# Optimization experiments

Hardware: AMD Instinct MI355X
Metric: run time of the kernel (lower is better)

The kernel has to match this reference:

```python
import jax, jax.numpy as jnp
import numpy as np

NB, H, C = 6, 4, 192
B, S, L = 2, 64, 256
VOCAB, ED = 24, 64


def setup_inputs() -> dict:
    key = jax.random.key(0)
    ks = iter(jax.random.split(key, 32))
    r = lambda sh: jax.random.normal(next(ks), sh, jnp.float32) * 0.02
    z = lambda sh: jnp.zeros(sh, jnp.float32)
    return {
        'tokens': jax.random.randint(next(ks), (B, S, L), 0, VOCAB, jnp.int32),
        'emb': r((VOCAB, ED)),
        'proj_w': r((C, ED)), 'proj_b': z((C,)),
        'ln_g': jnp.ones((NB, 3, C), jnp.float32), 'ln_b': z((NB, 3, C)),
        'wq': r((NB, 2, C, C)), 'wk': r((NB, 2, C, C)),
        'wv': r((NB, 2, C, C)), 'wo': r((NB, 2, C, C)),
        'bq': z((NB, 2, C)), 'bk': z((NB, 2, C)),
        'bv': z((NB, 2, C)), 'bo': z((NB, 2, C)),
        'ffn_w1': r((NB, 4 * C, C)), 'ffn_b1': z((NB, 4 * C)),
        'ffn_w2': r((NB, C, 4 * C)), 'ffn_b2': z((NB, C)),
        'pw_w': r((C,)), 'pw_b': z(()),
    }


def rotary(x):
    # ESM-style rotary embedding over positions along dim -2, feature dim last.
    d = x.shape[-1]
    inv = 1.0 / (10000.0 ** (jnp.arange(0, d, 2, dtype=jnp.float32) / d))
    t = jnp.arange(x.shape[-2], dtype=jnp.float32)
    f = t[:, None] * inv[None, :]                  # (pos, d/2)
    emb = jnp.concatenate([f, f], axis=-1)         # (pos, d)
    cos, sin = jnp.cos(emb), jnp.sin(emb)
    x1, x2 = jnp.split(x, 2, axis=-1)
    return x * cos + jnp.concatenate([-x2, x1], axis=-1) * sin


def ln_ch(x, g, b, eps=1e-5):
    # LayerNorm over channel axis 1 of (B,C,X,Y) (== transpose->LN->transpose).
    m = x.mean(axis=1, keepdims=True)
    v = jnp.var(x, axis=1, keepdims=True)
    return (x - m) * jax.lax.rsqrt(v + eps) * g[None, :, None, None] + b[None, :, None, None]


def lin_attn(x, wq, wk, wv, wo, bq, bk, bv, bo):
    # ScaledLinearAttention: elu+1 feature map, attends over dim -2 of (B,A,N,C).
    Bm, A, N, Cm = x.shape
    dh = Cm // H
    sh = lambda t: t.reshape(Bm, A, N, H, dh).transpose(0, 1, 3, 2, 4)  # (B,A,H,N,dh)
    q = sh(x @ wq.T + bq)
    k = sh(x @ wk.T + bk)
    v = sh(x @ wv.T + bv)
    q = (jax.nn.elu(q) + 1.0) / jnp.sqrt(jnp.float32(dh))
    k = jax.nn.elu(k) + 1.0
    kv = jnp.einsum('bahnd,bahne->bahde', k, v)
    z = 1.0 / (jnp.einsum('bahnd,bahd->bahn', q, k.sum(axis=-2)) + 1e-6)
    o = jnp.einsum('bahnd,bahde->bahne', q, kv) * z[..., None]
    o = o.transpose(0, 1, 3, 2, 4).reshape(Bm, A, N, Cm)
    return o @ wo.T + bo


def fwd(tokens, emb, proj_w, proj_b, ln_g, ln_b, wq, wk, wv, wo, bq, bk, bv, bo,
        ffn_w1, ffn_b1, ffn_w2, ffn_b2, pw_w, pw_b):
    x = emb[tokens]                    # (B,S,L,ED)
    x = x @ proj_w.T + proj_b          # (B,S,L,C)
    x = rotary(x)                      # rotary over L positions
    out = jnp.transpose(x, (0, 3, 1, 2))  # (B,C,S,L)
    for i in range(NB):
        # row attention (over L)
        h = ln_ch(out, ln_g[i, 0], ln_b[i, 0])
        h = jnp.transpose(h, (0, 2, 3, 1))  # (B,S,L,C)
        h = lin_attn(h, wq[i, 0], wk[i, 0], wv[i, 0], wo[i, 0],
                     bq[i, 0], bk[i, 0], bv[i, 0], bo[i, 0])
        out = out + jnp.transpose(h, (0, 3, 1, 2))
        # col attention (over S)
        h = ln_ch(out, ln_g[i, 1], ln_b[i, 1])
        h = jnp.transpose(h, (0, 3, 2, 1))  # (B,L,S,C)
        h = lin_attn(h, wq[i, 1], wk[i, 1], wv[i, 1], wo[i, 1],
                     bq[i, 1], bk[i, 1], bv[i, 1], bo[i, 1])
        out = out + jnp.transpose(h, (0, 3, 2, 1))
        # 1x1-conv FFN
        h = ln_ch(out, ln_g[i, 2], ln_b[i, 2])
        h = jnp.einsum('bcxy,oc->boxy', h, ffn_w1[i]) + ffn_b1[i][None, :, None, None]
        h = jax.nn.gelu(h, approximate=False)
        h = jnp.einsum('bcxy,oc->boxy', h, ffn_w2[i]) + ffn_b2[i][None, :, None, None]
        out = out + h
    o = jnp.einsum('bcxy,c->bxy', out, pw_w) + pw_b   # pwFNN 1x1 conv to 1 ch
    return jax.nn.sigmoid(jax.nn.softplus(o))


def reference(tokens, emb, proj_w, proj_b, ln_g, ln_b, wq, wk, wv, wo, bq, bk, bv, bo,
              ffn_w1, ffn_b1, ffn_w2, ffn_b2, pw_w, pw_b):
    return fwd(tokens, emb, proj_w, proj_b, ln_g, ln_b, wq, wk, wv, wo, bq, bk, bv, bo,
               ffn_w1, ffn_b1, ffn_w2, ffn_b2, pw_w, pw_b)
```

## Files before the change

### kernel.cpp

```cpp
#include <hip/hip_runtime.h>
#include <hip/hip_bf16.h>
#include <math.h>

#define NBLK 6
#define NH 4
#define CCH 192
#define BB 2
#define SS 64
#define LL 256
#define DH 48
#define NP (BB*SS*LL)
#define BUF ((size_t)NP*CCH)

typedef __attribute__((ext_vector_type(8))) short short8;
typedef __attribute__((ext_vector_type(4))) float float4v;
typedef __attribute__((ext_vector_type(2))) unsigned int uintx2;

__device__ __forceinline__ unsigned short f2b(float f) {
    union { float f; unsigned int u; } v; v.f = f;
    unsigned int r = v.u + 0x7FFF + ((v.u >> 16) & 1);
    return (unsigned short)(r >> 16);
}
__device__ __forceinline__ float b2f(unsigned short u) {
    union { unsigned int u; float f; } v; v.u = ((unsigned int)u) << 16;
    return v.f;
}
__device__ __forceinline__ unsigned int cvt_pk_bf16(float lo, float hi) {
    unsigned int r;
    asm("v_cvt_pk_bf16_f32 %0, %1, %2" : "=v"(r) : "v"(lo), "v"(hi));
    return r;
}
__device__ __forceinline__ void st2u(unsigned short* p0, unsigned short* p1, float a, float b) {
    unsigned int u = cvt_pk_bf16(a, b);
    *p0 = (unsigned short)u;
    *p1 = (unsigned short)(u >> 16);
}
__device__ __forceinline__ void xf_unpack(uintx2 u, float* f) {
    union { unsigned int x; float ff; } t;
    t.x = u[0] << 16;          f[0] = t.ff;
    t.x = u[0] & 0xffff0000u;  f[1] = t.ff;
    t.x = u[1] << 16;          f[2] = t.ff;
    t.x = u[1] & 0xffff0000u;  f[3] = t.ff;
}
__device__ __forceinline__ float gelu_f(float v) {
    float z = v * 0.7071067811865475f;
    float a = fabsf(z);
    float t = __builtin_amdgcn_rcpf(fmaf(0.3275911f, a, 1.0f));
    float p = fmaf(t, 1.061405429f, -1.453152027f);
    p = fmaf(t, p, 1.421413741f);
    p = fmaf(t, p, -0.284496736f);
    p = fmaf(t, p, 0.254829592f);
    p *= t;
    float e = __expf(-a * a);
    float er = fmaf(-p, e, 1.0f);
    er = __builtin_copysignf(er, z);
    return 0.5f * v * (1.0f + er);
}
__device__ __forceinline__ void async_lds16(const void* g, void* l) {
    __builtin_amdgcn_global_load_lds(
        (const __attribute__((address_space(1))) unsigned int*)g,
        (__attribute__((address_space(3))) unsigned int*)l, 16, 0, 0);
}

#define XF(p16, c) (((size_t)(p16) * 192 + (c)) << 4)

template<int N, int K>
__global__ void swz_conv(const float* __restrict__ src, unsigned short* __restrict__ dst, int layers) {
    int s = blockIdx.x * 256 + threadIdx.x;
    if (s >= layers * N * K) return;
    int li = s / (N * K);
    int t = s - li * (N * K);
    constexpr int KC = K / 32;
    int chunk = t >> 9, c = t & 511;
    int g = chunk / KC, sk = chunk - g * KC;
    int lane = c >> 3, ko = c & 7;
    int n = g * 16 + (lane & 15), k = sk * 32 + (lane >> 4) * 8 + ko;
    dst[s] = f2b(src[(size_t)li * N * K + (size_t)n * K + k]);
}
__global__ void wqkv_swz(const float* __restrict__ wq, const float* __restrict__ wk,
                         const float* __restrict__ wv, unsigned short* __restrict__ d) {
    int s = blockIdx.x * 256 + threadIdx.x;
    int wi = s / (576 * 192);
    int t = s - wi * 576 * 192;
    int chunk = t >> 9, c = t & 511;
    int g = chunk / 6, sk = chunk - g * 6;
    int lane = c >> 3, ko = c & 7;
    int n = g * 16 + (lane & 15), k = sk * 32 + (lane >> 4) * 8 + ko;
    int sg = n / 192, row = n - sg * 192;
    const float* src = (sg == 0) ? wq : (sg == 1) ? wk : wv;
    d[s] = f2b(src[(size_t)wi * 192 * 192 + (size_t)row * 192 + k]);
}
__global__ void bqkv_concat(const float* __restrict__ bq, const float* __restrict__ bk,
                            const float* __restrict__ bv, float* __restrict__ d) {
    int idx = blockIdx.x * 256 + threadIdx.x;
    if (idx >= NBLK * 2 * 576) return;
    int wi = idx / 576, n = idx - (idx / 576) * 576;
    int sg = n / 192, row = n - sg * 192;
    const float* src = (sg == 0) ? bq : (sg == 1) ? bk : bv;
    d[idx] = src[wi * CCH + row];
}

__global__ void gather_kernel(const int* __restrict__ tokens, const float* __restrict__ emb,
                              unsigned short* __restrict__ Eg) {
    int idx = blockIdx.x * 256 + threadIdx.x;
    int p = idx >> 6, c = idx & 63;
    Eg[idx] = f2b(emb[tokens[p] * 64 + c]);
}

__global__ __launch_bounds__(256) void rotary_ln_kernel(const float* __restrict__ Xt,
                                                        unsigned short* __restrict__ X,
                                                        unsigned short* __restrict__ Hn,
                                                        const float* __restrict__ g, const float* __restrict__ b) {
    int wave = threadIdx.x >> 6;
    int lane = threadIdx.x & 63;
    int p = blockIdx.x * 4 + wave;
    int l = p & (LL - 1);
    const float* xp = Xt + (size_t)p * CCH;
    float v[3];
    #pragma unroll
    for (int i = 0; i < 3; ++i) {
        int c = lane + i * 64;
        int j = c % 96;
        float inv = expf((float)(2 * j) * (-9.210340371976184f / 192.0f));
        float ang = (float)l * inv;
        float part = (c < 96) ? -xp[c + 96] : xp[c - 96];
        v[i] = xp[c] * cosf(ang) + part * sinf(ang);
    }
    float s = v[0] + v[1] + v[2];
    float qq = v[0] * v[0] + v[1] * v[1] + v[2] * v[2];
    #pragma unroll
    for (int off = 32; off; off >>= 1) {
        s += __shfl_xor(s, off, 64);
        qq += __shfl_xor(qq, off, 64);
    }
    float mean = s * (1.0f / 192.0f);
    float var = qq * (1.0f / 192.0f) - mean * mean;
    float r = rsqrtf(var + 1e-5f);
    unsigned short* hp = Hn + (size_t)p * CCH;
    const int p16 = p >> 4, pr = p & 15;
    #pragma unroll
    for (int i = 0; i < 3; ++i) {
        int c = lane + i * 64;
        X[XF(p16, c) + pr] = f2b(v[i]);
        hp[c] = f2b((v[i] - mean) * r * g[c] + b[c]);
    }
}

template<int MT, int EPI>
__global__ __launch_bounds__(256, (MT == 128) ? 3 : 4)
void mm192(const unsigned short* __restrict__ A, const unsigned short* __restrict__ Wsw,
           const float* __restrict__ bias,
           unsigned short* __restrict__ O0, unsigned short* __restrict__ O1,
           unsigned short* __restrict__ O2,
           float* __restrict__ Of,
           int M, int N, int K) {
    constexpr int NI = MT / 32;
    __shared__ __align__(16) unsigned char lds[(MT == 128) ? 51200 : 28672];
    const int tid = threadIdx.x;
    const int lane = tid & 63;
    const int w = tid >> 6;
    const int wm = w >> 1, wn = w & 1;
    const int m0 = blockIdx.y * MT;
    const int g0 = blockIdx.x * 12;
    const int q = lane >> 4;
    const int q8 = q << 3;
    const int r15 = lane & 15;
    const int KC = K >> 5;

    for (int c = w; c < (MT / 16) * KC; c += 4) {
        int g = c / KC, sk = c - g * KC;
        async_lds16(A + (size_t)(m0 + g * 16 + r15) * K + sk * 32 + q8, lds + c * 1024);
    }

    float4v acc[NI][6];
    #pragma unroll
    for (int i = 0; i < NI; ++i)
        #pragma unroll
        for (int j = 0; j < 6; ++j)
            acc[i][j] = (float4v){0.f, 0.f, 0.f, 0.f};

    __syncthreads();

    for (int sk = 0; sk < KC; ++sk) {
        short8 af[NI], wf[6];
        #pragma unroll
        for (int j = 0; j < 6; ++j)
            wf[j] = *(const short8*)(Wsw + (((size_t)(g0 + wn * 6 + j) * KC + sk) << 9) + lane * 8);
        #pragma unroll
        for (int i = 0; i < NI; ++i)
            af[i] = *(const short8*)(lds + (((wm * NI + i) * KC + sk) << 10) + lane * 16);
        #pragma unroll
        for (int i = 0; i < NI; ++i)
            #pragma unroll
            for (int j = 0; j < 6; ++j)
                acc[i][j] = __builtin_amdgcn_mfma_f32_16x16x32_bf16(af[i], wf[j], acc[i][j], 0, 0, 0);
    }

    const int nb = blockIdx.x * 192 + wn * 96 + r15;
    const int mb = m0 + wm * (MT / 2) + q * 4;

    if (EPI == 0) {
        const int bx = blockIdx.x;
        unsigned short* dst = (bx == 0) ? O0 : (bx == 1) ? O1 : O2;
        #pragma unroll
        for (int j = 0; j < 6; ++j) {
            int n = nb + j * 16;
            int col = wn * 96 + j * 16 + r15;
            float bv = bias[n];
            #pragma unroll
            for (int i = 0; i < NI; ++i) {
                int mrow = wm * (MT / 2) + i * 16 + q * 4;
                #pragma unroll
                for (int r = 0; r < 4; ++r) {
                    float v = acc[i][j][r] + bv;
                    if (bx < 2) v = (v > 0.f) ? v + 1.f : __expf(v);
                    if (bx == 0) v *= 0.14433756729740643f;
                    dst[(size_t)(m0 + mrow + r) * 192 + col] = f2b(v);
                }
            }
        }
    } else {
        #pragma unroll
        for (int j = 0; j < 6; ++j) {
            int n = nb + j * 16;
            float bv = bias[n];
            #pragma unroll
            for (int i = 0; i < NI; ++i) {
                int mrow = mb + i * 16;
                #pragma unroll
                for (int r = 0; r < 4; ++r)
                    Of[(size_t)(mrow + r) * N + n] = acc[i][j][r] + bv;
            }
        }
    }
}


__global__ __launch_bounds__(256, 4)
void wo_qkv(const unsigned short* __restrict__ Ho,
            const unsigned short* __restrict__ WOs, const float* __restrict__ BO,
            unsigned short* __restrict__ Xres,
            const float* __restrict__ lng, const float* __restrict__ lnb,
            const unsigned short* __restrict__ QKVs, const float* __restrict__ bqkv,
            unsigned short* __restrict__ Qb, unsigned short* __restrict__ Kb,
            unsigned short* __restrict__ Vb) {
    __shared__ __align__(16) unsigned char lds[25600];
    unsigned char* Lo = lds;
    float* lsum = (float*)(lds + 12288);
    float* lsq  = lsum + 128;
    unsigned char* Ap = lds + 13312;
    const int tid = threadIdx.x;
    const int lane = tid & 63;
    const int w = tid >> 6;
    const int m0 = blockIdx.x * 32;
    const int q = lane >> 4, q8 = q << 3, r15 = lane & 15;
    const int nb = w * 48 + r15;

    #pragma unroll
    for (int it = 0; it < 3; ++it) {
        int c = it * 4 + w;
        int g = c / 6, sk = c - g * 6;
        async_lds16(Ho + (size_t)(m0 + g * 16 + r15) * 192 + sk * 32 + q8, Lo + c * 1024);
    }
    __syncthreads();

    float4v acc[2][3];
    #pragma unroll
    for (int i = 0; i < 2; ++i)
        #pragma unroll
        for (int j = 0; j < 3; ++j)
            acc[i][j] = (float4v){0.f, 0.f, 0.f, 0.f};
    #pragma unroll
    for (int kk = 0; kk < 6; ++kk) {
        short8 af[2], wf[3];
        #pragma unroll
        for (int j = 0; j < 3; ++j)
            wf[j] = *(const short8*)(WOs + (((size_t)(w * 3 + j) * 6 + kk) << 9) + lane * 8);
        #pragma unroll
        for (int i = 0; i < 2; ++i)
            af[i] = *(const short8*)(Lo + ((i * 6 + kk) << 10) + lane * 16);
        #pragma unroll
        for (int i = 0; i < 2; ++i)
            #pragma unroll
            for (int j = 0; j < 3; ++j)
                acc[i][j] = __builtin_amdgcn_mfma_f32_16x16x32_bf16(af[i], wf[j], acc[i][j], 0, 0, 0);
    }

    #pragma unroll
    for (int j = 0; j < 3; ++j) {
        int n = nb + j * 16;
        float bv = BO[n];
        #pragma unroll
        for (int i = 0; i < 2; ++i) {
            unsigned short* xp = Xres + XF(blockIdx.x * 2 + i, n) + q * 4;
            uintx2 u = *(const uintx2*)xp;
            float f[4]; xf_unpack(u, f);
            #pragma unroll
            for (int r = 0; r < 4; ++r) acc[i][j][r] += bv + f[r];
            uintx2 o;
            o[0] = cvt_pk_bf16(acc[i][j][0], acc[i][j][1]);
            o[1] = cvt_pk_bf16(acc[i][j][2], acc[i][j][3]);
            *(uintx2*)xp = o;
        }
    }
    #pragma unroll
    for (int i = 0; i < 2; ++i)
        #pragma unroll
        for (int r = 0; r < 4; ++r) {
            float s1 = acc[i][0][r] + acc[i][1][r] + acc[i][2][r];
            float s2 = acc[i][0][r] * acc[i][0][r] + acc[i][1][r] * acc[i][1][r] + acc[i][2][r] * acc[i][2][r];
            #pragma unroll
            for (int off = 1; off < 16; off <<= 1) {
                s1 += __shfl_xor(s1, off, 64);
                s2 += __shfl_xor(s2, off, 64);
            }
            if (r15 == 0) {
                int rl = i * 16 + q * 4 + r;
                lsum[rl * 4 + w] = s1;
                lsq[rl * 4 + w] = s2;
            }
        }
    __syncthreads();
    #pragma unroll
    for (int i = 0; i < 2; ++i) {
        float mean[4], rstd[4];
        #pragma unroll
        for (int r = 0; r < 4; ++r) {
            int rl4 = (i * 16 + q * 4 + r) * 4;
            float s  = lsum[rl4] + lsum[rl4 + 1] + lsum[rl4 + 2] + lsum[rl4 + 3];
            float ss = lsq[rl4] + lsq[rl4 + 1] + lsq[rl4 + 2] + lsq[rl4 + 3];
            float m = s * (1.0f / 192.0f);
            mean[r] = m;
            rstd[r] = rsqrtf(ss * (1.0f / 192.0f) - m * m + 1e-5f);
        }
        #pragma unroll
        for (int j = 0; j < 3; ++j) {
            int h = nb + j * 16;
            float gg = lng[h], bb = lnb[h];
            unsigned short* ap = (unsigned short*)Ap + (i * 6 + (h >> 5)) * 512
                               + ((h >> 3) & 3) * 128 + (h & 7) + q * 32;
            float v0 = (acc[i][j][0] - mean[0]) * rstd[0] * gg + bb;
            float v1 = (acc[i][j][1] - mean[1]) * rstd[1] * gg + bb;
            float v2 = (acc[i][j][2] - mean[2]) * rstd[2] * gg + bb;
            float v3 = (acc[i][j][3] - mean[3]) * rstd[3] * gg + bb;
            st2u(ap, ap + 8, v0, v1);
            st2u(ap + 16, ap + 24, v2, v3);
        }
    }
    __syncthreads();

    for (int seg = 0; seg < 3; ++seg) {
        float4v a2[2][3];
        #pragma unroll
        for (int i = 0; i < 2; ++i)
            #pragma unroll
            for (int j = 0; j < 3; ++j)
                a2[i][j] = (float4v){0.f, 0.f, 0.f, 0.f};
        #pragma unroll
        for (int kk = 0; kk < 6; ++kk) {
            short8 af[2], wf[3];
            #pragma unroll
            for (int j = 0; j < 3; ++j)
                wf[j] = *(const short8*)(QKVs + (((size_t)(seg * 12 + w * 3 + j) * 6 + kk) << 9) + lane * 8);
            #pragma unroll
            for (int i = 0; i < 2; ++i)
                af[i] = *(const short8*)(Ap + ((i * 6 + kk) << 10) + lane * 16);
            #pragma unroll
            for (int i = 0; i < 2; ++i)
                #pragma unroll
                for (int j = 0; j < 3; ++j)
                    a2[i][j] = __builtin_amdgcn_mfma_f32_16x16x32_bf16(af[i], wf[j], a2[i][j], 0, 0, 0);
        }
        unsigned short* dst = (seg == 0) ? Qb : (seg == 1) ? Kb : Vb;
        #pragma unroll
        for (int j = 0; j < 3; ++j) {
            int n = nb + j * 16;
            float bv = bqkv[seg * 192 + n];
            #pragma unroll
            for (int i = 0; i < 2; ++i) {
                int mrow = m0 + i * 16 + q * 4;
                #pragma unroll
                for (int r = 0; r < 4; ++r) {
                    float x = a2[i][j][r] + bv;
                    if (seg < 2) x = (x > 0.f) ? x + 1.f : __expf(x);
                    if (seg == 0) x *= 0.14433756729740643f;
                    dst[(size_t)(mrow + r) * 192 + n] = f2b(x);
                }
            }
        }
    }
}

template<bool LASTB>
__global__ __launch_bounds__(256, 2)
void wo_ffn_qkv(const unsigned short* __restrict__ Ho,
                const unsigned short* __restrict__ WOs, const float* __restrict__ BO,
                unsigned short* __restrict__ Xres,
                const float* __restrict__ ln1g, const float* __restrict__ ln1b,
                const unsigned short* __restrict__ W1s, const float* __restrict__ B1,
                const unsigned short* __restrict__ W2s, const float* __restrict__ B2,
                const float* __restrict__ ln2g, const float* __restrict__ ln2b,
                const unsigned short* __restrict__ QKVs, const float* __restrict__ bqkv,
                unsigned short* __restrict__ Qb, unsigned short* __restrict__ Kb,
                unsigned short* __restrict__ Vb) {
    __shared__ __align__(16) unsigned char lds[51200];
    unsigned char* Lo = lds;
    float* lsum = (float*)(lds + 24576);
    float* lsq  = lsum + 256;
    unsigned char* Ap = lds + 26624;
    const int tid = threadIdx.x;
    const int lane = tid & 63;
    const int w = tid >> 6;
    const int m0 = blockIdx.x * 64;
    const int q = lane >> 4, q8 = q << 3, r15 = lane & 15;
    const int nb = w * 48 + r15;

    #pragma unroll
    for (int it = 0; it < 6; ++it) {
        int c = it * 4 + w;
        int g = c / 6, sk = c - g * 6;
        async_lds16(Ho + (size_t)(m0 + g * 16 + r15) * 192 + sk * 32 + q8, Lo + c * 1024);
    }
    __syncthreads();

    float4v xres[4][3];
    #pragma unroll
    for (int i = 0; i < 4; ++i)
        #pragma unroll
        for (int j = 0; j < 3; ++j)
            xres[i][j] = (float4v){0.f, 0.f, 0.f, 0.f};
    #pragma unroll
    for (int kk = 0; kk < 6; ++kk) {
        short8 af[4], wf[3];
        #pragma unroll
        for (int j = 0; j < 3; ++j)
            wf[j] = *(const short8*)(WOs + (((size_t)(w * 3 + j) * 6 + kk) << 9) + lane * 8);
        #pragma unroll
        for (int i = 0; i < 4; ++i)
            af[i] = *(const short8*)(Lo + ((i * 6 + kk) << 10) + lane * 16);
        #pragma unroll
        for (int i = 0; i < 4; ++i)
            #pragma unroll
            for (int j = 0; j < 3; ++j)
                xres[i][j] = __builtin_amdgcn_mfma_f32_16x16x32_bf16(af[i], wf[j], xres[i][j], 0, 0, 0);
    }
    #pragma unroll
    for (int j = 0; j < 3; ++j) {
        int n = nb + j * 16;
        float bv = BO[n];
        #pragma unroll
        for (int i = 0; i < 4; ++i) {
            const unsigned short* xp = Xres + XF(blockIdx.x * 4 + i, n) + q * 4;
            uintx2 u = *(const uintx2*)xp;
            float f[4]; xf_unpack(u, f);
            #pragma unroll
            for (int r = 0; r < 4; ++r) xres[i][j][r] += bv + f[r];
        }
    }
    #pragma unroll
    for (int i = 0; i < 4; ++i)
        #pragma unroll
        for (int r = 0; r < 4; ++r) {
            float s1 = xres[i][0][r] + xres[i][1][r] + xres[i][2][r];
            float s2 = xres[i][0][r] * xres[i][0][r] + xres[i][1][r] * xres[i][1][r] + xres[i][2][r] * xres[i][2][r];
            #pragma unroll
            for (int off = 1; off < 16; off <<= 1) {
                s1 += __shfl_xor(s1, off, 64);
                s2 += __shfl_xor(s2, off, 64);
            }
            if (r15 == 0) {
                int rl = i * 16 + q * 4 + r;
                lsum[rl * 4 + w] = s1;
                lsq[rl * 4 + w] = s2;
            }
        }
    __syncthreads();
    #pragma unroll
    for (int i = 0; i < 4; ++i) {
        float mean[4], rstd[4];
        #pragma unroll
        for (int r = 0; r < 4; ++r) {
            int rl4 = (i * 16 + q * 4 + r) * 4;
            float s  = lsum[rl4] + lsum[rl4 + 1] + lsum[rl4 + 2] + lsum[rl4 + 3];
            float ss = lsq[rl4] + lsq[rl4 + 1] + lsq[rl4 + 2] + lsq[rl4 + 3];
            float m = s * (1.0f / 192.0f);
            mean[r] = m;
            rstd[r] = rsqrtf(ss * (1.0f / 192.0f) - m * m + 1e-5f);
        }
        #pragma unroll
        for (int j = 0; j < 3; ++j) {
            int h = nb + j * 16;
            float gg = ln1g[h], bb = ln1b[h];
            unsigned short* ap = (unsigned short*)Ap + (i * 6 + (h >> 5)) * 512
                               + ((h >> 3) & 3) * 128 + (h & 7) + q * 32;
            float v0 = (xres[i][j][0] - mean[0]) * rstd[0] * gg + bb;
            float v1 = (xres[i][j][1] - mean[1]) * rstd[1] * gg + bb;
            float v2 = (xres[i][j][2] - mean[2]) * rstd[2] * gg + bb;
            float v3 = (xres[i][j][3] - mean[3]) * rstd[3] * gg + bb;
            st2u(ap, ap + 8, v0, v1);
            st2u(ap + 16, ap + 24, v2, v3);
        }
    }
    __syncthreads();

    float4v acc2[4][3];
    #pragma unroll
    for (int i = 0; i < 4; ++i)
        #pragma unroll
        for (int j = 0; j < 3; ++j)
            acc2[i][j] = (float4v){0.f, 0.f, 0.f, 0.f};
    for (int hc = 0; hc < 4; ++hc) {
        float4v acc1[4][3];
        #pragma unroll
        for (int i = 0; i < 4; ++i)
            #pragma unroll
            for (int j = 0; j < 3; ++j)
                acc1[i][j] = (float4v){0.f, 0.f, 0.f, 0.f};
        #pragma unroll
        for (int kk = 0; kk < 6; ++kk) {
            short8 af[4], wf[3];
            #pragma unroll
            for (int j = 0; j < 3; ++j)
                wf[j] = *(const short8*)(W1s + (((size_t)(hc * 12 + w * 3 + j) * 6 + kk) << 9) + lane * 8);
            #pragma unroll
            for (int i = 0; i < 4; ++i)
                af[i] = *(const short8*)(Ap + ((i * 6 + kk) << 10) + lane * 16);
            #pragma unroll
            for (int i = 0; i < 4; ++i)
                #pragma unroll
                for (int j = 0; j < 3; ++j)
                    acc1[i][j] = __builtin_amdgcn_mfma_f32_16x16x32_bf16(af[i], wf[j], acc1[i][j], 0, 0, 0);
        }
        __syncthreads();
        #pragma unroll
        for (int i = 0; i < 4; ++i)
            #pragma unroll
            for (int j = 0; j < 3; ++j) {
                int h = nb + j * 16;
                float bv = B1[hc * 192 + h];
                unsigned short* lp = (unsigned short*)Lo + (i * 6 + (h >> 5)) * 512
                                   + ((h >> 3) & 3) * 128 + (h & 7) + q * 32;
                float v0 = gelu_f(acc1[i][j][0] + bv);
                float v1 = gelu_f(acc1[i][j][1] + bv);
                float v2 = gelu_f(acc1[i][j][2] + bv);
                float v3 = gelu_f(acc1[i][j][3] + bv);
                st2u(lp, lp + 8, v0, v1);
                st2u(lp + 16, lp + 24, v2, v3);
            }
        __syncthreads();
        #pragma unroll
        for (int kk = 0; kk < 6; ++kk) {
            short8 af[4], wf[3];
            #pragma unroll
            for (int j = 0; j < 3; ++j)
                wf[j] = *(const short8*)(W2s + (((size_t)(w * 3 + j) * 24 + hc * 6 + kk) << 9) + lane * 8);
            #pragma unroll
            for (int i = 0; i < 4; ++i)
                af[i] = *(const short8*)(Lo + ((i * 6 + kk) << 10) + lane * 16);
            #pragma unroll
            for (int i = 0; i < 4; ++i)
                #pragma unroll
                for (int j = 0; j < 3; ++j)
                    acc2[i][j] = __builtin_amdgcn_mfma_f32_16x16x32_bf16(af[i], wf[j], acc2[i][j], 0, 0, 0);
        }
    }

    #pragma unroll
    for (int j = 0; j < 3; ++j) {
        int n = nb + j * 16;
        float bv = B2[n];
        #pragma unroll
        for (int i = 0; i < 4; ++i) {
            #pragma unroll
            for (int r = 0; r < 4; ++r)
                xres[i][j][r] += acc2[i][j][r] + bv;
            unsigned short* xp = Xres + XF(blockIdx.x * 4 + i, n) + q * 4;
            uintx2 o;
            o[0] = cvt_pk_bf16(xres[i][j][0], xres[i][j][1]);
            o[1] = cvt_pk_bf16(xres[i][j][2], xres[i][j][3]);
            *(uintx2*)xp = o;
        }
    }
    if (LASTB) return;

    #pragma unroll
    for (int i = 0; i < 4; ++i)
        #pragma unroll
        for (int r = 0; r < 4; ++r) {
            float s1 = xres[i][0][r] + xres[i][1][r] + xres[i][2][r];
            float s2 = xres[i][0][r] * xres[i][0][r] + xres[i][1][r] * xres[i][1][r] + xres[i][2][r] * xres[i][2][r];
            #pragma unroll
            for (int off = 1; off < 16; off <<= 1) {
                s1 += __shfl_xor(s1, off, 64);
                s2 += __shfl_xor(s2, off, 64);
            }
            if (r15 == 0) {
                int rl = i * 16 + q * 4 + r;
                lsum[rl * 4 + w] = s1;
                lsq[rl * 4 + w] = s2;
            }
        }
    __syncthreads();
    #pragma unroll
    for (int i = 0; i < 4; ++i) {
        float mean[4], rstd[4];
        #pragma unroll
        for (int r = 0; r < 4; ++r) {
            int rl4 = (i * 16 + q * 4 + r) * 4;
            float s  = lsum[rl4] + lsum[rl4 + 1] + lsum[rl4 + 2] + lsum[rl4 + 3];
            float ss = lsq[rl4] + lsq[rl4 + 1] + lsq[rl4 + 2] + lsq[rl4 + 3];
            float m = s * (1.0f / 192.0f);
            mean[r] = m;
            rstd[r] = rsqrtf(ss * (1.0f / 192.0f) - m * m + 1e-5f);
        }
        #pragma unroll
        for (int j = 0; j < 3; ++j) {
            int h = nb + j * 16;
            float gg = ln2g[h], bb = ln2b[h];
            unsigned short* ap = (unsigned short*)Ap + (i * 6 + (h >> 5)) * 512
                               + ((h >> 3) & 3) * 128 + (h & 7) + q * 32;
            float v0 = (xres[i][j][0] - mean[0]) * rstd[0] * gg + bb;
            float v1 = (xres[i][j][1] - mean[1]) * rstd[1] * gg + bb;
            float v2 = (xres[i][j][2] - mean[2]) * rstd[2] * gg + bb;
            float v3 = (xres[i][j][3] - mean[3]) * rstd[3] * gg + bb;
            st2u(ap, ap + 8, v0, v1);
            st2u(ap + 16, ap + 24, v2, v3);
        }
    }
    __syncthreads();

    for (int seg = 0; seg < 3; ++seg) {
        float4v a2[4][3];
        #pragma unroll
        for (int i = 0; i < 4; ++i)
            #pragma unroll
            for (int j = 0; j < 3; ++j)
                a2[i][j] = (float4v){0.f, 0.f, 0.f, 0.f};
        #pragma unroll
        for (int kk = 0; kk < 6; ++kk) {
            short8 af[4], wf[3];
            #pragma unroll
            for (int j = 0; j < 3; ++j)
                wf[j] = *(const short8*)(QKVs + (((size_t)(seg * 12 + w * 3 + j) * 6 + kk) << 9) + lane * 8);
            #pragma unroll
            for (int i = 0; i < 4; ++i)
                af[i] = *(const short8*)(Ap + ((i * 6 + kk) << 10) + lane * 16);
            #pragma unroll
            for (int i = 0; i < 4; ++i)
                #pragma unroll
                for (int j = 0; j < 3; ++j)
                    a2[i][j] = __builtin_amdgcn_mfma_f32_16x16x32_bf16(af[i], wf[j], a2[i][j], 0, 0, 0);
        }
        unsigned short* dst = (seg == 0) ? Qb : (seg == 1) ? Kb : Vb;
        #pragma unroll
        for (int j = 0; j < 3; ++j) {
            int n = nb + j * 16;
            float bv = bqkv[seg * 192 + n];
            #pragma unroll
            for (int i = 0; i < 4; ++i) {
                int mrow = m0 + i * 16 + q * 4;
                #pragma unroll
                for (int r = 0; r < 4; ++r) {
                    float x = a2[i][j][r] + bv;
                    if (seg < 2) x = (x > 0.f) ? x + 1.f : __expf(x);
                    if (seg == 0) x *= 0.14433756729740643f;
                    dst[(size_t)(mrow + r) * 192 + n] = f2b(x);
                }
            }
        }
    }
}

__global__ __launch_bounds__(512) void attn_row8(const unsigned short* __restrict__ Qb,
                                                 const unsigned short* __restrict__ Kb,
                                                 const unsigned short* __restrict__ Vb,
                                                 unsigned short* __restrict__ O) {
    __shared__ __align__(16) unsigned char lds[100352];
    unsigned char* kvb = lds;
    float* kvsum = (float*)(lds + 51200);
    unsigned short* kvs = (unsigned short*)lds;
    const int tid = threadIdx.x;
    const int lane = tid & 63;
    const int w = tid >> 6;
    const int h = w & 3;
    const int half = w >> 2;
    const int q = lane >> 4, r15 = lane & 15, q8 = q * 8;
    const size_t base = (size_t)blockIdx.x * 256;

    short8 onesf;
    #pragma unroll
    for (int e = 0; e < 8; ++e) onesf[e] = (short)0x3F80;

    float4v kv[3][4];
    #pragma unroll
    for (int i = 0; i < 3; ++i)
        #pragma unroll
        for (int j = 0; j < 4; ++j)
            kv[i][j] = (float4v){0.f, 0.f, 0.f, 0.f};

    for (int ks = 0; ks < 128; ks += 32) {
        #pragma unroll
        for (int it = 0; it < 6; ++it) {
            int cc = it * 512 + tid;
            int gr = cc / 48, c8 = cc - gr * 48;
            int hf = gr >> 5, row = gr & 31;
            size_t poff = (base + (size_t)(ks + hf * 128 + row)) * 192;
            const unsigned short* gp = (c8 < 24) ? (Kb + poff + c8 * 8) : (Vb + poff + (c8 - 24) * 8);
            int ba = hf * 25600 + ((row * 800 + c8 * 16) ^ (((row >> 3) & 3) << 5));
            *(short8*)(kvb + ba) = *(const short8*)gp;
        }
        __syncthreads();
        short8 af[3], bf[3];
        const unsigned char* hb = kvb + half * 25600;
        #pragma unroll
        for (int t = 0; t < 3; ++t) {
            #pragma unroll
            for (int j = 0; j < 8; ++j) {
                int row = q8 + j;
                int sw = ((row >> 3) & 3) << 5;
                af[t][j] = *(const short*)(hb + ((row * 800 + (h * 48 + t * 16 + r15) * 2) ^ sw));
                bf[t][j] = *(const short*)(hb + ((row * 800 + 384 + (h * 48 + t * 16 + r15) * 2) ^ sw));
            }
        }
        #pragma unroll
        for (int i = 0; i < 3; ++i) {
            #pragma unroll
            for (int j = 0; j < 3; ++j)
                kv[i][j] = __builtin_amdgcn_mfma_f32_16x16x32_bf16(af[i], bf[j], kv[i][j], 0, 0, 0);
            kv[i][3] = __builtin_amdgcn_mfma_f32_16x16x32_bf16(af[i], onesf, kv[i][3], 0, 0, 0);
        }
        __syncthreads();
    }

    if (half) {
        float* kp = kvsum + h * 3072;
        #pragma unroll
        for (int i = 0; i < 3; ++i)
            #pragma unroll
            for (int j = 0; j < 4; ++j)
                #pragma unroll
                for (int r = 0; r < 4; ++r)
                    kp[((i * 4 + j) * 4 + r) * 64 + lane] = kv[i][j][r];
    }
    __syncthreads();
    if (!half) {
        const float* kp = kvsum + h * 3072;
        #pragma unroll
        for (int i = 0; i < 3; ++i)
            #pragma unroll
            for (int j = 0; j < 4; ++j)
                #pragma unroll
                for (int r = 0; r < 4; ++r)
                    kv[i][j][r] += kp[((i * 4 + j) * 4 + r) * 64 + lane];
        unsigned int* kz = (unsigned int*)(kvs + h * 4608);
        #pragma unroll
        for (int ii = 0; ii < 36; ++ii) kz[lane + ii * 64] = 0;
        #pragma unroll
        for (int i = 0; i < 3; ++i) {
            #pragma unroll
            for (int j = 0; j < 3; ++j)
                #pragma unroll
                for (int r = 0; r < 4; ++r)
                    kvs[(h * 64 + j * 16 + r15) * 72 + i * 16 + q * 4 + r] = f2b(kv[i][j][r]);
            if (r15 == 0)
                #pragma unroll
                for (int r = 0; r < 4; ++r)
                    kvs[(h * 64 + 48) * 72 + i * 16 + q * 4 + r] = f2b(kv[i][3][r]);
        }
    }
    __syncthreads();

    short8 bkv[2][4];
    #pragma unroll
    for (int kk = 0; kk < 2; ++kk)
        #pragma unroll
        for (int t = 0; t < 4; ++t)
            bkv[kk][t] = *(const short8*)&kvs[(h * 64 + t * 16 + r15) * 72 + kk * 32 + q8];

    for (int mt = half * 8; mt < half * 8 + 8; ++mt) {
        float4v o[4];
        #pragma unroll
        for (int t = 0; t < 4; ++t) o[t] = (float4v){0.f, 0.f, 0.f, 0.f};
        #pragma unroll
        for (int kk = 0; kk < 2; ++kk) {
            const unsigned short* qp = Qb + (base + (size_t)(mt * 16 + r15)) * 192
                                       + h * 48 + kk * 32 + q8;
            short8 aq = *(const short8*)qp;
            #pragma unroll
            for (int t = 0; t < 4; ++t)
                o[t] = __builtin_amdgcn_mfma_f32_16x16x32_bf16(aq, bkv[kk][t], o[t], 0, 0, 0);
        }
        #pragma unroll
        for (int r = 0; r < 4; ++r) {
            float den = __shfl(o[3][r], q << 4);
            float z = 1.0f / (den + 1e-6f);
            int n = mt * 16 + q * 4 + r;
            unsigned short* op = O + (base + (size_t)n) * 192 + h * 48;
            #pragma unroll
            for (int t = 0; t < 3; ++t)
                op[t * 16 + r15] = f2b(o[t][r] * z);
        }
    }
}

template<int N, int MSTR>
__global__ __launch_bounds__(256) void attn_axial(const unsigned short* __restrict__ Qb,
                                                  const unsigned short* __restrict__ Kb,
                                                  const unsigned short* __restrict__ Vb,
                                                  unsigned short* __restrict__ O) {
    __shared__ unsigned short KV[32][400];
    __shared__ unsigned short kvs[4][64][72];
    unsigned char* kvb = (unsigned char*)KV;
    const int tid = threadIdx.x;
    const int lane = tid & 63;
    const int w = tid >> 6;
    const int q = lane >> 4, r15 = lane & 15, q8 = q * 8;
    size_t base;
    if (MSTR == 1) base = (size_t)blockIdx.x * N;
    else           base = (size_t)(blockIdx.x >> 8) * 16384 + (blockIdx.x & 255);

    unsigned int* kz = (unsigned int*)&kvs[w][0][0];
    #pragma unroll
    for (int ii = 0; ii < 36; ++ii) kz[lane + ii * 64] = 0;

    short8 onesf;
    #pragma unroll
    for (int e = 0; e < 8; ++e) onesf[e] = (short)0x3F80;

    float4v kv[3][4];
    #pragma unroll
    for (int i = 0; i < 3; ++i)
        #pragma unroll
        for (int j = 0; j < 4; ++j)
            kv[i][j] = (float4v){0.f, 0.f, 0.f, 0.f};

    for (int ks = 0; ks < N; ks += 32) {
        #pragma unroll
        for (int it = 0; it < 6; ++it) {
            int cc = tid + it * 256;
            int row = cc / 48, c8 = cc - (cc / 48) * 48;
            size_t poff = (base + (size_t)(ks + row) * MSTR) * 192;
            const unsigned short* gp = (c8 < 24) ? (Kb + poff + c8 * 8) : (Vb + poff + (c8 - 24) * 8);
            int ba = (row * 800 + c8 * 16) ^ (((row >> 3) & 3) << 5);
            *(short8*)(kvb + ba) = *(const short8*)gp;
        }
        __syncthreads();
        short8 af[3], bf[3];
        #pragma unroll
        for (int t = 0; t < 3; ++t) {
            #pragma unroll
            for (int j = 0; j < 8; ++j) {
                int row = q8 + j;
                int sw = ((row >> 3) & 3) << 5;
                af[t][j] = *(short*)(kvb + ((row * 800 + (w * 48 + t * 16 + r15) * 2) ^ sw));
                bf[t][j] = *(short*)(kvb + ((row * 800 + 384 + (w * 48 + t * 16 + r15) * 2) ^ sw));
            }
        }
        #pragma unroll
        for (int i = 0; i < 3; ++i) {
            #pragma unroll
            for (int j = 0; j < 3; ++j)
                kv[i][j] = __builtin_amdgcn_mfma_f32_16x16x32_bf16(af[i], bf[j], kv[i][j], 0, 0, 0);
            kv[i][3] = __builtin_amdgcn_mfma_f32_16x16x32_bf16(af[i], onesf, kv[i][3], 0, 0, 0);
        }
        __syncthreads();
    }

    #pragma unroll
    for (int i = 0; i < 3; ++i) {
        #pragma unroll
        for (int j = 0; j < 3; ++j)
            #pragma unroll
            for (int r = 0; r < 4; ++r)
                kvs[w][j * 16 + r15][i * 16 + q * 4 + r] = f2b(kv[i][j][r]);
        if (r15 == 0)
            #pragma unroll
            for (int r = 0; r < 4; ++r)
                kvs[w][48][i * 16 + q * 4 + r] = f2b(kv[i][3][r]);
    }

    short8 bkv[2][4];
    #pragma unroll
    for (int kk = 0; kk < 2; ++kk)
        #pragma unroll
        for (int t = 0; t < 4; ++t)
            bkv[kk][t] = *(const short8*)&kvs[w][t * 16 + r15][kk * 32 + q8];

    for (int mt = 0; mt < N / 16; ++mt) {
        float4v o[4];
        #pragma unroll
        for (int t = 0; t < 4; ++t) o[t] = (float4v){0.f, 0.f, 0.f, 0.f};
        #pragma unroll
        for (int kk = 0; kk < 2; ++kk) {
            const unsigned short* qp = Qb + (base + (size_t)(mt * 16 + r15) * MSTR) * 192
                                       + w * 48 + kk * 32 + q8;
            short8 aq = *(const short8*)qp;
            #pragma unroll
            for (int t = 0; t < 4; ++t)
                o[t] = __builtin_amdgcn_mfma_f32_16x16x32_bf16(aq, bkv[kk][t], o[t], 0, 0, 0);
        }
        #pragma unroll
        for (int r = 0; r < 4; ++r) {
            float den = __shfl(o[3][r], q << 4);
            float z = 1.0f / (den + 1e-6f);
            int n = mt * 16 + q * 4 + r;
            unsigned short* op = O + (base + (size_t)n * MSTR) * 192 + w * 48;
            #pragma unroll
            for (int t = 0; t < 3; ++t)
                op[t * 16 + r15] = f2b(o[t][r] * z);
        }
    }
}

__global__ __launch_bounds__(256) void final_kernel(const unsigned short* __restrict__ X,
                                                    const float* __restrict__ pw_w,
                                                    const float* __restrict__ pw_b, float* __restrict__ out) {
    int wave = threadIdx.x >> 6;
    int lane = threadIdx.x & 63;
    int p = blockIdx.x * 4 + wave;
    const unsigned short* xp = X + XF(p >> 4, 0) + (p & 15);
    float s = b2f(xp[(size_t)lane << 4]) * pw_w[lane]
            + b2f(xp[(size_t)(lane + 64) << 4]) * pw_w[lane + 64]
            + b2f(xp[(size_t)(lane + 128) << 4]) * pw_w[lane + 128];
    #pragma unroll
    for (int off = 32; off; off >>= 1) s += __shfl_xor(s, off, 64);
    if (lane == 0) {
        float o = s + pw_b[0];
        float e = expf(o);
        out[p] = 1.0f - 1.0f / (2.0f + e);
    }
}

extern "C" void kernel_launch(void* const* d_in, const int* in_sizes, int n_in,
                              void* d_out, int out_size, void* d_ws, size_t ws_size,
                              hipStream_t stream) {
    const int*   tokens = (const int*)  d_in[0];
    const float* emb    = (const float*)d_in[1];
    const float* proj_w = (const float*)d_in[2];
    const float* proj_b = (const float*)d_in[3];
    const float* ln_g   = (const float*)d_in[4];
    const float* ln_b   = (const float*)d_in[5];
    const float* wq     = (const float*)d_in[6];
    const float* wk     = (const float*)d_in[7];
    const float* wv     = (const float*)d_in[8];
    const float* wo     = (const float*)d_in[9];
    const float* bq     = (const float*)d_in[10];
    const float* bk     = (const float*)d_in[11];
    const float* bv     = (const float*)d_in[12];
    const float* bo     = (const float*)d_in[13];
    const float* ffn_w1 = (const float*)d_in[14];
    const float* ffn_b1 = (const float*)d_in[15];
    const float* ffn_w2 = (const float*)d_in[16];
    const float* ffn_b2 = (const float*)d_in[17];
    const float* pw_w   = (const float*)d_in[18];
    const float* pw_b   = (const float*)d_in[19];

    unsigned short* X    = (unsigned short*)d_ws;
    unsigned short* Ho   = X + BUF;
    unsigned short* Qb   = Ho + BUF;
    unsigned short* Kb   = Qb + BUF;
    unsigned short* Vb   = Kb + BUF;
    unsigned short* Eg   = Vb + BUF;
    unsigned short* wqkvb = Eg + (size_t)NP * 64;
    const int QKVSZ = NBLK * 2 * 576 * CCH;
    const int WSZ   = NBLK * 2 * CCH * CCH;
    const int FSZ   = NBLK * 768 * CCH;
    unsigned short* wob = wqkvb + QKVSZ;
    unsigned short* w1b = wob + WSZ;
    unsigned short* w2b = w1b + FSZ;
    unsigned short* pjb = w2b + FSZ;
    float* bqkvb = (float*)(pjb + 12288 + 32);
    float* Xt = (float*)Qb;

    wqkv_swz<<<QKVSZ / 256, 256, 0, stream>>>(wq, wk, wv, wqkvb);
    bqkv_concat<<<27, 256, 0, stream>>>(bq, bk, bv, bqkvb);
    swz_conv<192, 192><<<(WSZ + 255) / 256, 256, 0, stream>>>(wo, wob, NBLK * 2);
    swz_conv<768, 192><<<(FSZ + 255) / 256, 256, 0, stream>>>(ffn_w1, w1b, NBLK);
    swz_conv<192, 768><<<(FSZ + 255) / 256, 256, 0, stream>>>(ffn_w2, w2b, NBLK);
    swz_conv<192, 64><<<48, 256, 0, stream>>>(proj_w, pjb, 1);

    gather_kernel<<<NP * 64 / 256, 256, 0, stream>>>(tokens, emb, Eg);
    mm192<64, 1><<<dim3(1, NP / 64), 256, 0, stream>>>(Eg, pjb, proj_b,
                                                       nullptr, nullptr, nullptr, Xt, NP, CCH, 64);
    rotary_ln_kernel<<<NP / 4, 256, 0, stream>>>(Xt, X, Ho, ln_g, ln_b);
    mm192<128, 0><<<dim3(3, NP / 128), 256, 0, stream>>>(Ho, wqkvb, bqkvb,
                                                         Qb, Kb, Vb, nullptr, NP, 576, CCH);

    for (int i = 0; i < NBLK; ++i) {
        size_t wi0 = (size_t)(i * 2), wi1 = wi0 + 1;
        attn_row8<<<BB * SS, 512, 0, stream>>>(Qb, Kb, Vb, Ho);
        wo_qkv<<<NP / 32, 256, 0, stream>>>(Ho, wob + wi0 * CCH * CCH, bo + wi0 * CCH, X,
                                            ln_g + (size_t)(i * 3 + 1) * CCH, ln_b + (size_t)(i * 3 + 1) * CCH,
                                            wqkvb + wi1 * 576 * CCH, bqkvb + wi1 * 576, Qb, Kb, Vb);
        attn_axial<SS, LL><<<BB * LL, 256, 0, stream>>>(Qb, Kb, Vb, Ho);
        if (i < NBLK - 1) {
            size_t wn0 = (size_t)((i + 1) * 2);
            wo_ffn_qkv<false><<<NP / 64, 256, 0, stream>>>(
                Ho, wob + wi1 * CCH * CCH, bo + wi1 * CCH, X,
                ln_g + (size_t)(i * 3 + 2) * CCH, ln_b + (size_t)(i * 3 + 2) * CCH,
                w1b + (size_t)i * 768 * CCH, ffn_b1 + (size_t)i * 768,
                w2b + (size_t)i * CCH * 768, ffn_b2 + (size_t)i * CCH,
                ln_g + (size_t)((i + 1) * 3) * CCH, ln_b + (size_t)((i + 1) * 3) * CCH,
                wqkvb + wn0 * 576 * CCH, bqkvb + wn0 * 576, Qb, Kb, Vb);
        } else {
            wo_ffn_qkv<true><<<NP / 64, 256, 0, stream>>>(
                Ho, wob + wi1 * CCH * CCH, bo + wi1 * CCH, X,
                ln_g + (size_t)(i * 3 + 2) * CCH, ln_b + (size_t)(i * 3 + 2) * CCH,
                w1b + (size_t)i * 768 * CCH, ffn_b1 + (size_t)i * 768,
                w2b + (size_t)i * CCH * 768, ffn_b2 + (size_t)i * CCH,
                nullptr, nullptr, nullptr, nullptr, nullptr, nullptr, nullptr);
        }
    }
    final_kernel<<<NP / 4, 256, 0, stream>>>(X, pw_w, pw_b, (float*)d_out);
}
```

Before: 875.4 us.

## Split row attention into one block per head with single-shot K/V staging

The row linear-attention kernel now launches one 256-thread block per (row, head) instead of one 512-thread block per row covering all four heads, which gives four times as many blocks. Each block loads only its head's 48-wide K/V slice for all 256 positions in one register-staged pass. This replaces the four-iteration load loop that had a sync on every iteration. The four waves each accumulate a 64-position slice of KV and then reduce through LDS with a four-way sum. The goal is better occupancy and fewer barriers, paid for by more blocks and an extra cross-wave reduction.

```diff
diff --git a/kernel.cpp b/kernel.cpp
--- a/kernel.cpp
+++ b/kernel.cpp
@@ -671,21 +671,39 @@
     }
 }
 
-__global__ __launch_bounds__(512) void attn_row8(const unsigned short* __restrict__ Qb,
+__global__ __launch_bounds__(256) void attn_rowh(const unsigned short* __restrict__ Qb,
                                                  const unsigned short* __restrict__ Kb,
                                                  const unsigned short* __restrict__ Vb,
                                                  unsigned short* __restrict__ O) {
-    __shared__ __align__(16) unsigned char lds[100352];
-    unsigned char* kvb = lds;
-    float* kvsum = (float*)(lds + 51200);
-    unsigned short* kvs = (unsigned short*)lds;
+    __shared__ __align__(16) unsigned char lds[58368];
+    unsigned char* stg = lds;
+    float* pub = (float*)lds;
+    unsigned short* kvs = (unsigned short*)(lds + 49152);
     const int tid = threadIdx.x;
     const int lane = tid & 63;
-    const int w = tid >> 6;
-    const int h = w & 3;
-    const int half = w >> 2;
+    const int wq = tid >> 6;
+    const int h = blockIdx.x & 3;
+    const size_t base = (size_t)(blockIdx.x >> 2) * 256;
     const int q = lane >> 4, r15 = lane & 15, q8 = q * 8;
-    const size_t base = (size_t)blockIdx.x * 256;
+
+    short8 rg[12];
+    #pragma unroll
+    for (int it = 0; it < 12; ++it) {
+        int u = it * 256 + tid;
+        int row = u / 12, c8 = u - (u / 12) * 12;
+        const unsigned short* gp = (c8 < 6)
+            ? (Kb + (base + row) * 192 + h * 48 + c8 * 8)
+            : (Vb + (base + row) * 192 + h * 48 + (c8 - 6) * 8);
+        rg[it] = *(const short8*)gp;
+    }
+    #pragma unroll
+    for (int it = 0; it < 12; ++it) {
+        int u = it * 256 + tid;
+        int row = u / 12, c8 = u - (u / 12) * 12;
+        int ba = (row * 208 + c8 * 16) ^ (((row >> 3) & 3) << 5);
+        *(short8*)(stg + ba) = rg[it];
+    }
+    __syncthreads();
 
     short8 onesf;
     #pragma unroll
@@ -698,28 +716,18 @@
         for (int j = 0; j < 4; ++j)
             kv[i][j] = (float4v){0.f, 0.f, 0.f, 0.f};
 
-    for (int ks = 0; ks < 128; ks += 32) {
-        #pragma unroll
-        for (int it = 0; it < 6; ++it) {
-            int cc = it * 512 + tid;
-            int gr = cc / 48, c8 = cc - gr * 48;
-            int hf = gr >> 5, row = gr & 31;
-            size_t poff = (base + (size_t)(ks + hf * 128 + row)) * 192;
-            const unsigned short* gp = (c8 < 24) ? (Kb + poff + c8 * 8) : (Vb + poff + (c8 - 24) * 8);
-            int ba = hf * 25600 + ((row * 800 + c8 * 16) ^ (((row >> 3) & 3) << 5));
-            *(short8*)(kvb + ba) = *(const short8*)gp;
-        }
-        __syncthreads();
+    #pragma unroll
+    for (int sc = 0; sc < 2; ++sc) {
+        int ks0 = wq * 64 + sc * 32;
         short8 af[3], bf[3];
-        const unsigned char* hb = kvb + half * 25600;
         #pragma unroll
         for (int t = 0; t < 3; ++t) {
             #pragma unroll
             for (int j = 0; j < 8; ++j) {
-                int row = q8 + j;
+                int row = ks0 + q8 + j;
                 int sw = ((row >> 3) & 3) << 5;
-                af[t][j] = *(const short*)(hb + ((row * 800 + (h * 48 + t * 16 + r15) * 2) ^ sw));
-                bf[t][j] = *(const short*)(hb + ((row * 800 + 384 + (h * 48 + t * 16 + r15) * 2) ^ sw));
+                af[t][j] = *(const short*)(stg + ((row * 208 + (t * 16 + r15) * 2) ^ sw));
+                bf[t][j] = *(const short*)(stg + ((row * 208 + 96 + (t * 16 + r15) * 2) ^ sw));
             }
         }
         #pragma unroll
@@ -729,11 +737,11 @@
                 kv[i][j] = __builtin_amdgcn_mfma_f32_16x16x32_bf16(af[i], bf[j], kv[i][j], 0, 0, 0);
             kv[i][3] = __builtin_amdgcn_mfma_f32_16x16x32_bf16(af[i], onesf, kv[i][3], 0, 0, 0);
         }
-        __syncthreads();
-    }
-
-    if (half) {
-        float* kp = kvsum + h * 3072;
+    }
+    __syncthreads();
+
+    {
+        float* kp = pub + wq * 3072;
         #pragma unroll
         for (int i = 0; i < 3; ++i)
             #pragma unroll
@@ -743,31 +751,28 @@
                     kp[((i * 4 + j) * 4 + r) * 64 + lane] = kv[i][j][r];
     }
     __syncthreads();
-    if (!half) {
-        const float* kp = kvsum + h * 3072;
-        #pragma unroll
-        for (int i = 0; i < 3; ++i)
-            #pragma unroll
-            for (int j = 0; j < 4; ++j)
-                #pragma unroll
-                for (int r = 0; r < 4; ++r)
-                    kv[i][j][r] += kp[((i * 4 + j) * 4 + r) * 64 + lane];
-        unsigned int* kz = (unsigned int*)(kvs + h * 4608);
-        #pragma unroll
-        for (int ii = 0; ii < 36; ++ii) kz[lane + ii * 64] = 0;
-        #pragma unroll
-        for (int i = 0; i < 3; ++i) {
-            #pragma unroll
-            for (int j = 0; j < 3; ++j)
-                #pragma unroll
-                for (int r = 0; r < 4; ++r)
-                    kvs[(h * 64 + j * 16 + r15) * 72 + i * 16 + q * 4 + r] = f2b(kv[i][j][r]);
-            if (r15 == 0)
-                #pragma unroll
-                for (int r = 0; r < 4; ++r)
-                    kvs[(h * 64 + 48) * 72 + i * 16 + q * 4 + r] = f2b(kv[i][3][r]);
-        }
-    }
+
+    {
+        unsigned int* kz = (unsigned int*)kvs;
+        #pragma unroll
+        for (int z = 0; z < 2; ++z) {
+            int zz = z * 256 + tid;
+            int zr = zz >> 3, zc = zz & 7;
+            kz[zr * 36 + 24 + zc] = 0;
+        }
+    }
+    #pragma unroll
+    for (int i = 0; i < 3; ++i)
+        #pragma unroll
+        for (int r = 0; r < 4; ++r) {
+            int idx = ((i * 4 + wq) * 4 + r) * 64 + lane;
+            float s = pub[idx] + pub[3072 + idx] + pub[6144 + idx] + pub[9216 + idx];
+            int kc = i * 16 + q * 4 + r;
+            if (wq < 3)
+                kvs[(wq * 16 + r15) * 72 + kc] = f2b(s);
+            else
+                kvs[(48 + r15) * 72 + kc] = (r15 == 0) ? f2b(s) : (unsigned short)0;
+        }
     __syncthreads();
 
     short8 bkv[2][4];
@@ -775,9 +780,11 @@
     for (int kk = 0; kk < 2; ++kk)
         #pragma unroll
         for (int t = 0; t < 4; ++t)
-            bkv[kk][t] = *(const short8*)&kvs[(h * 64 + t * 16 + r15) * 72 + kk * 32 + q8];
-
-    for (int mt = half * 8; mt < half * 8 + 8; ++mt) {
+            bkv[kk][t] = *(const short8*)&kvs[(t * 16 + r15) * 72 + kk * 32 + q8];
+
+    #pragma unroll
+    for (int m = 0; m < 4; ++m) {
+        int mt = wq * 4 + m;
         float4v o[4];
         #pragma unroll
         for (int t = 0; t < 4; ++t) o[t] = (float4v){0.f, 0.f, 0.f, 0.f};
@@ -988,7 +995,7 @@
 
     for (int i = 0; i < NBLK; ++i) {
         size_t wi0 = (size_t)(i * 2), wi1 = wi0 + 1;
-        attn_row8<<<BB * SS, 512, 0, stream>>>(Qb, Kb, Vb, Ho);
+        attn_rowh<<<BB * SS * 4, 256, 0, stream>>>(Qb, Kb, Vb, Ho);
         wo_qkv<<<NP / 32, 256, 0, stream>>>(Ho, wob + wi0 * CCH * CCH, bo + wi0 * CCH, X,
                                             ln_g + (size_t)(i * 3 + 1) * CCH, ln_b + (size_t)(i * 3 + 1) * CCH,
                                             wqkvb + wi1 * 576 * CCH, bqkvb + wi1 * 576, Qb, Kb, Vb);
```

After: 854.2 us (median of 3 runs). 2.4% less time.
